# Performance work log

Hardware: AMD Instinct MI355X
Metric: run time of the kernel (lower is better)

## Reference

```python
import jax, jax.numpy as jnp
import numpy as np

B, N, F, U = 16, 2048, 64, 64

def setup_inputs() -> dict:
    key = jax.random.key(0)
    k1, k2, k3 = jax.random.split(key, 3)
    node_features = jax.random.normal(k1, (B, N, F), dtype=jnp.float32)
    adjacency_matrix = (jax.random.uniform(k2, (B, N, N)) < 0.01).astype(jnp.float32)
    kernel = jax.random.normal(k3, (F, U), dtype=jnp.float32) * (1.0 / np.sqrt(F))
    return {"node_features": node_features, "adjacency_matrix": adjacency_matrix, "kernel": kernel}

def reference(node_features, adjacency_matrix, kernel):
    # A_tilde = A + I  (self-loops)
    n = adjacency_matrix.shape[-1]
    adj = adjacency_matrix + jnp.eye(n, dtype=adjacency_matrix.dtype)
    # symmetric normalization D^-1/2 A_tilde D^-1/2 (diag matmuls == broadcast scaling)
    row_sum = jnp.sum(adj, axis=-1)                      # [B, N]
    d_inv_sqrt = jnp.where(row_sum > 0, row_sum ** -0.5, 0.0)
    norm_adj = d_inv_sqrt[:, :, None] * adj * d_inv_sqrt[:, None, :]
    # feature transform then aggregate, fused with ReLU
    transformed = jnp.einsum('bnf,fu->bnu', node_features, kernel)
    out = jnp.einsum('bnm,bmu->bnu', norm_adj, transformed)
    return jax.nn.relu(out)
```

## Files before the change

### kernel.cpp

```cpp
#include <hip/hip_runtime.h>
#include <hip/hip_bf16.h>


#define NB     16
#define NN     2048
#define NF     64
#define NU     64
#define NROWS  (NB * NN)
#define NGRP   (NROWS / 4)
#define K2BLK  2048
#define K2IT   (NGRP / K2BLK)

typedef unsigned int uint;
typedef uint vuint4 __attribute__((ext_vector_type(4)));

__device__ __forceinline__ int map_row(int g, int wid) {
    const int x = g & 7, s = g >> 3;
    const int batch = x + ((s >> 9) << 3);
    const int grp = s & 511;
    return (batch << 11) + (grp << 2) + wid;
}

__global__ __launch_bounds__(256) void k1_rowsum_compact(
    const float* __restrict__ A, float* __restrict__ d,
    int* __restrict__ counts, int* __restrict__ idx, int cap)
{
    const int t = threadIdx.x, wid = t >> 6, lane = t & 63;
    const int row = map_row(blockIdx.x, wid);
    const uint* Arow = reinterpret_cast<const uint*>(A + (size_t)row * NN);
    const unsigned long long lmask_lt = (lane == 63) ? 0x7fffffffffffffffull
                                                     : ((1ull << lane) - 1ull);
    vuint4 a[8];
    #pragma unroll
    for (int c = 0; c < 8; ++c)
        a[c] = __builtin_nontemporal_load(
            reinterpret_cast<const vuint4*>(Arow) + c * 64 + lane);

    const size_t base = (size_t)row * cap;
    int cnt = 0;
    #pragma unroll
    for (int c = 0; c < 8; ++c) {
        #pragma unroll
        for (int e = 0; e < 4; ++e) {
            const bool nz = (a[c][e] != 0u);
            const unsigned long long m = __ballot(nz);
            if (m) {
                if (nz) {
                    const int slot = cnt + __popcll(m & lmask_lt);
                    if (slot < cap)
                        idx[base + slot] = ((c * 64 + lane) << 2) + e;
                }
                cnt += __popcll(m);
            }
        }
    }
    if (lane == 0) {
        d[row]      = rsqrtf((float)cnt + 1.0f);
        counts[row] = cnt;
    }
}

__global__ __launch_bounds__(256) void k2_transform_scale(
    const float* __restrict__ X, const float* __restrict__ W,
    const float* __restrict__ d, float* __restrict__ Tp)
{
    const int t = threadIdx.x, wid = t >> 6, lane = t & 63;
    float wcol[NF];
    #pragma unroll
    for (int f = 0; f < NF; ++f) wcol[f] = W[f * NU + lane];

    #pragma unroll
    for (int it = 0; it < K2IT; ++it) {
        const int g   = blockIdx.x + it * K2BLK;
        const int row = map_row(g, wid);
        const float xv = X[(size_t)row * NF + lane];
        const float dr = d[row];
        float acc = 0.f;
        #pragma unroll
        for (int f = 0; f < NF; ++f) {
            const float xf = __int_as_float(
                __builtin_amdgcn_readlane(__float_as_int(xv), f));
            acc += xf * wcol[f];
        }
        Tp[(size_t)row * NU + lane] = acc * dr;
    }
}

__global__ __launch_bounds__(256) void k3_aggregate(
    const float* __restrict__ A, const float* __restrict__ Tp,
    const float* __restrict__ d, const int* __restrict__ counts,
    const int* __restrict__ idx, float* __restrict__ out, int cap)
{
    const int t = threadIdx.x, wid = t >> 6, lane = t & 63;
    const int row = map_row(blockIdx.x, wid);
    const int b   = row >> 11;
    const float* Tb = Tp + (((size_t)b) << 11) * NU;

    float a0 = Tp[(size_t)row * NU + lane];
    float a1 = 0.f;
    const int cnt = counts[row];
    if (cnt <= cap) {
        const size_t base = (size_t)row * cap;
        const int4* q4 = reinterpret_cast<const int4*>(idx + base);
        const int nfull = cnt >> 2;
        if (nfull > 0) {
            int4 qq = q4[0];
            for (int q = 0; q < nfull; ++q) {
                const int4 cur = qq;
                if (q + 1 < nfull) qq = q4[q + 1];
                const float t0 = Tb[((size_t)(uint)cur.x << 6) + lane];
                const float t1 = Tb[((size_t)(uint)cur.y << 6) + lane];
                const float t2 = Tb[((size_t)(uint)cur.z << 6) + lane];
                const float t3 = Tb[((size_t)(uint)cur.w << 6) + lane];
                a0 += t0 + t2;
                a1 += t1 + t3;
            }
        }
        for (int k = nfull << 2; k < cnt; ++k)
            a1 += Tb[((size_t)(uint)idx[base + k] << 6) + lane];
    } else {
        const float* Arow = A + (size_t)row * NN;
        for (int j = 0; j < NN; ++j)
            if (Arow[j] != 0.f) a1 += Tb[((size_t)j << 6) + lane];
    }
    const float r = d[row] * (a0 + a1);
    __builtin_nontemporal_store(r > 0.f ? r : 0.f,
                                &out[(size_t)row * NU + lane]);
}

extern "C" void kernel_launch(void* const* d_in, const int* in_sizes, int n_in,
                              void* d_out, int out_size, void* d_ws, size_t ws_size,
                              hipStream_t stream)
{
    const float* X = (const float*)d_in[0];
    const float* A = (const float*)d_in[1];
    const float* W = (const float*)d_in[2];
    float* out = (float*)d_out;

    char* ws = (char*)d_ws;
    float* Tp     = (float*)ws;
    float* dvec   = (float*)(ws + (size_t)NROWS * NU * 4);
    int*   counts = (int*)  (ws + (size_t)NROWS * NU * 4 + (size_t)NROWS * 4);
    int*   idx    = (int*)  (ws + (size_t)NROWS * NU * 4 + 2ull * NROWS * 4);

    const size_t fixed = (size_t)NROWS * NU * 4 + 2ull * NROWS * 4;
    int cap = 0;
    if (ws_size > fixed) {
        size_t c = (ws_size - fixed) / ((size_t)NROWS * sizeof(int));
        cap = (int)(c < 128 ? c : 128);
        cap &= ~3;
    }

    k1_rowsum_compact<<<NGRP, 256, 0, stream>>>(A, dvec, counts, idx, cap);
    k2_transform_scale<<<K2BLK, 256, 0, stream>>>(X, W, dvec, Tp);
    k3_aggregate<<<NGRP, 256, 0, stream>>>(A, Tp, dvec, counts, idx, out, cap);
}
```

Baseline: 372.9 us.

## Split adjacency compaction into bitmap pass and prefix-scan decode kernel

The streaming pass over the dense adjacency now only packs nonzero flags into a per-lane 32-bit bitmap, with no per-element ballots or scattered index writes. A new decode kernel reads the bitmap, does a wave prefix scan of popcounts, and writes the compacted column indices, counts and degree normalisation. The aim is to keep the memory-bound pass over the 268MB adjacency free of serialized ballot work. The cost is an extra launch and a 8MB bitmap round trip through memory, and the per-lane indices are no longer written in column order.

Result: no change. 380.2 us (+1.9%).

```diff
diff --git a/kernel.cpp b/kernel.cpp
--- a/kernel.cpp
+++ b/kernel.cpp
@@ -21,42 +21,53 @@
     return (batch << 11) + (grp << 2) + wid;
 }
 
-__global__ __launch_bounds__(256) void k1_rowsum_compact(
-    const float* __restrict__ A, float* __restrict__ d,
-    int* __restrict__ counts, int* __restrict__ idx, int cap)
+__global__ __launch_bounds__(256) void k1_bitmap(
+    const float* __restrict__ A, uint* __restrict__ bm)
 {
     const int t = threadIdx.x, wid = t >> 6, lane = t & 63;
     const int row = map_row(blockIdx.x, wid);
     const uint* Arow = reinterpret_cast<const uint*>(A + (size_t)row * NN);
-    const unsigned long long lmask_lt = (lane == 63) ? 0x7fffffffffffffffull
-                                                     : ((1ull << lane) - 1ull);
     vuint4 a[8];
     #pragma unroll
     for (int c = 0; c < 8; ++c)
         a[c] = __builtin_nontemporal_load(
             reinterpret_cast<const vuint4*>(Arow) + c * 64 + lane);
 
-    const size_t base = (size_t)row * cap;
-    int cnt = 0;
+    uint word = 0u;
     #pragma unroll
     for (int c = 0; c < 8; ++c) {
         #pragma unroll
-        for (int e = 0; e < 4; ++e) {
-            const bool nz = (a[c][e] != 0u);
-            const unsigned long long m = __ballot(nz);
-            if (m) {
-                if (nz) {
-                    const int slot = cnt + __popcll(m & lmask_lt);
-                    if (slot < cap)
-                        idx[base + slot] = ((c * 64 + lane) << 2) + e;
-                }
-                cnt += __popcll(m);
-            }
-        }
+        for (int e = 0; e < 4; ++e)
+            word |= (a[c][e] != 0u) ? (1u << (c * 4 + e)) : 0u;
     }
-    if (lane == 0) {
-        d[row]      = rsqrtf((float)cnt + 1.0f);
-        counts[row] = cnt;
+    bm[(size_t)row * 64 + lane] = word;
+}
+
+__global__ __launch_bounds__(256) void k1b_decode(
+    const uint* __restrict__ bm, float* __restrict__ d,
+    int* __restrict__ counts, int* __restrict__ idx, int cap)
+{
+    const int t = threadIdx.x, wid = t >> 6, lane = t & 63;
+    const int row = map_row(blockIdx.x, wid);
+    uint w = bm[(size_t)row * 64 + lane];
+    const int nl = __popc(w);
+    int incl = nl;
+    #pragma unroll
+    for (int o = 1; o < 64; o <<= 1) {
+        const int v = __shfl_up(incl, o);
+        incl = (lane >= o) ? incl + v : incl;
+    }
+    int p = incl - nl;
+    const size_t base = (size_t)row * cap;
+    while (w) {
+        const int b = __builtin_ctz(w); w &= w - 1;
+        const int j = ((b >> 2) << 8) + (lane << 2) + (b & 3);
+        if (p < cap) idx[base + p] = j;
+        ++p;
+    }
+    if (lane == 63) {
+        counts[row] = incl;
+        d[row]      = rsqrtf((float)incl + 1.0f);
     }
 }
 
@@ -138,20 +149,22 @@
     float* out = (float*)d_out;
 
     char* ws = (char*)d_ws;
-    float* Tp     = (float*)ws;
-    float* dvec   = (float*)(ws + (size_t)NROWS * NU * 4);
-    int*   counts = (int*)  (ws + (size_t)NROWS * NU * 4 + (size_t)NROWS * 4);
-    int*   idx    = (int*)  (ws + (size_t)NROWS * NU * 4 + 2ull * NROWS * 4);
+    size_t off = 0;
+    float* Tp     = (float*)(ws + off); off += (size_t)NROWS * NU * 4;
+    float* dvec   = (float*)(ws + off); off += (size_t)NROWS * 4;
+    int*   counts = (int*)  (ws + off); off += (size_t)NROWS * 4;
+    uint*  bm     = (uint*) (ws + off); off += (size_t)NROWS * 64 * 4;
+    int*   idx    = (int*)  (ws + off);
 
-    const size_t fixed = (size_t)NROWS * NU * 4 + 2ull * NROWS * 4;
     int cap = 0;
-    if (ws_size > fixed) {
-        size_t c = (ws_size - fixed) / ((size_t)NROWS * sizeof(int));
+    if (ws_size > off) {
+        size_t c = (ws_size - off) / ((size_t)NROWS * sizeof(int));
         cap = (int)(c < 128 ? c : 128);
         cap &= ~3;
     }
 
-    k1_rowsum_compact<<<NGRP, 256, 0, stream>>>(A, dvec, counts, idx, cap);
+    k1_bitmap   <<<NGRP, 256, 0, stream>>>(A, bm);
+    k1b_decode  <<<NGRP, 256, 0, stream>>>(bm, dvec, counts, idx, cap);
     k2_transform_scale<<<K2BLK, 256, 0, stream>>>(X, W, dvec, Tp);
     k3_aggregate<<<NGRP, 256, 0, stream>>>(A, Tp, dvec, counts, idx, out, cap);
 }
```
